# Kernel optimization log

Hardware: AMD Instinct MI355X
Metric: run time of the kernel (lower is better)

Reference implementation:

```python
import jax, jax.numpy as jnp
import numpy as np

HEADS = 8

def setup_inputs() -> dict:
    key = jax.random.key(0)
    ks = jax.random.split(key, 6)
    N, C, L = 8, 512, 2048
    s = 0.02
    return {
        'x':  jax.random.normal(ks[0], (N, C, L), dtype=jnp.float32),
        'Wq': jax.random.normal(ks[1], (C, C), dtype=jnp.float32) * s,
        'Wk': jax.random.normal(ks[2], (C, C), dtype=jnp.float32) * s,
        'Wv': jax.random.normal(ks[3], (C, C), dtype=jnp.float32) * s,
        'Wo': jax.random.normal(ks[4], (C, C), dtype=jnp.float32) * s,
        'bo': jnp.zeros((C,), dtype=jnp.float32),
    }

def reference(x, Wq, Wk, Wv, Wo, bo):
    N, C, L = x.shape
    h = HEADS
    d = C // h
    scale = C ** (-0.5)  # note: scales by full channels, as in the original

    def proj(W):
        # Conv1d(k=1, bias=False) == per-position linear: [N,C,L] -> [N,L,h,d]
        y = jnp.einsum('oc,ncl->nlo', W, x)
        return y.reshape(N, L, h, d)

    q, k, v = proj(Wq), proj(Wk), proj(Wv)

    qk = jnp.einsum('nqhd,nkhd->nhqk', q, k)  # [N,h,L,L]
    causal_mask = jnp.tril(jnp.ones((L, L), dtype=bool))
    qk = jnp.where(causal_mask, qk, -jnp.inf)
    attn = jax.nn.softmax(qk * scale, axis=-1)

    out = jnp.einsum('nhqk,nkhd->nqhd', attn, v)  # [N,L,h,d]
    out = out.reshape(N, L, C).transpose(0, 2, 1)  # n (h d) l
    return jnp.einsum('oc,ncl->nol', Wo, out) + bo[None, :, None]
```

## Files before the change

### kernel.cpp

```cpp
#include <hip/hip_runtime.h>
#include <math.h>

typedef __bf16 bf16;
typedef __attribute__((ext_vector_type(8))) __bf16 bf16x8;
typedef __attribute__((ext_vector_type(4))) float f32x4;
typedef __attribute__((ext_vector_type(16))) float f32x16;
typedef unsigned short u16;
typedef unsigned int u32;

constexpr int Nn = 8, Cc = 512, Ll = 2048, Hh = 8, Dd = 64;
constexpr float kScale = 0.044194173824159216f;
constexpr float kQexp2 = kScale * 1.44269504088896341f;
constexpr size_t NCL = (size_t)Nn * Cc * Ll;
constexpr size_t WSZ = (size_t)Cc * Cc;

static __device__ __forceinline__ u16 bfbits(bf16 v) {
    union { bf16 b; u16 u; } x; x.b = v; return x.u;
}
static __device__ __forceinline__ float fexp2(float x) {
#if __has_builtin(__builtin_amdgcn_exp2f)
    return __builtin_amdgcn_exp2f(x);
#else
    return exp2f(x);
#endif
}

#define MFMA(a, b, c) __builtin_amdgcn_mfma_f32_16x16x32_bf16((a), (b), (c), 0, 0, 0)
#define MFMA32(a, b, c) __builtin_amdgcn_mfma_f32_32x32x16_bf16((a), (b), (c), 0, 0, 0)

static __device__ __forceinline__ void async16(const bf16* g, bf16* l) {
    __builtin_amdgcn_global_load_lds(
        (const __attribute__((address_space(1))) void*)g,
        (__attribute__((address_space(3))) void*)l, 16, 0, 0);
}

static __device__ __forceinline__ u32 cvtpk(float lo, float hi) {
    u32 d;
    asm("v_cvt_pk_bf16_f32 %0, %1, %2" : "=v"(d) : "v"(lo), "v"(hi));
    return d;
}
static __device__ __forceinline__ void swap32(u32& d, u32& s) {
    asm volatile("v_permlane32_swap_b32 %0, %1" : "+v"(d), "+v"(s));
}

__global__ __launch_bounds__(256) void prep_kernel(
    const float* __restrict__ x,
    const float* __restrict__ Wq, const float* __restrict__ Wk,
    const float* __restrict__ Wv, const float* __restrict__ Wo,
    bf16* __restrict__ xT, bf16* __restrict__ Wb)
{
    const int tid = threadIdx.x;
    if (blockIdx.z == Nn) {
        int gid = (blockIdx.y * 32 + blockIdx.x) * 256 + tid;
        int w = gid >> 14;
        int o = (gid & 16383) * 4;
        const float* src = (w == 0) ? Wq : (w == 1) ? Wk : (w == 2) ? Wv : Wo;
        bf16* dst = Wb + (size_t)w * WSZ;
#pragma unroll
        for (int j = 0; j < 4; j++) {
            float4 v = ((const float4*)src)[o + j];
            ushort4 u;
            u.x = bfbits((bf16)v.x); u.y = bfbits((bf16)v.y);
            u.z = bfbits((bf16)v.z); u.w = bfbits((bf16)v.w);
            *(ushort4*)(dst + (size_t)(o + j) * 4) = u;
        }
        return;
    }

    __shared__ bf16 Ts[64][72];
    const int lt = blockIdx.x, ct = blockIdx.y, n = blockIdx.z;

    const int cr = tid >> 2, l0 = (tid & 3) * 16;
    const float* src = x + ((size_t)(n * Cc + ct * 64 + cr)) * Ll + lt * 64 + l0;
#pragma unroll
    for (int i = 0; i < 4; i++) {
        float4 v = *(const float4*)(src + i * 4);
        Ts[l0 + i * 4 + 0][cr] = (bf16)v.x;
        Ts[l0 + i * 4 + 1][cr] = (bf16)v.y;
        Ts[l0 + i * 4 + 2][cr] = (bf16)v.z;
        Ts[l0 + i * 4 + 3][cr] = (bf16)v.w;
    }
    __syncthreads();

    const int lr = tid >> 2, c0 = (tid & 3) * 16;
    bf16* dst = xT + ((size_t)(n * Ll + lt * 64 + lr)) * Cc + ct * 64 + c0;
    *(bf16x8*)(dst)     = *(const bf16x8*)&Ts[lr][c0];
    *(bf16x8*)(dst + 8) = *(const bf16x8*)&Ts[lr][c0 + 8];
}

__global__ __launch_bounds__(256) void qkv_gemm(
    const bf16* __restrict__ xT, const bf16* __restrict__ Wb,
    bf16* __restrict__ Qt, bf16* __restrict__ Kt, bf16* __restrict__ Vb)
{
    const int lt = blockIdx.x, ow = blockIdx.y, n = blockIdx.z;
    const int widx = ow >> 2, otile = ow & 3;

    __shared__ bf16 Xs[128 * 64];
    __shared__ bf16 Ws[128 * 64];

    const int tid = threadIdx.x;
    const int lane = tid & 63, wv = tid >> 6;
    const int m = lane & 15, quad = lane >> 4;
    const int rh = wv & 1, ch = wv >> 1;

    const bf16* __restrict__ W = Wb + (size_t)widx * WSZ + (size_t)otile * 128 * Cc;
    const bf16* __restrict__ X = xT + (size_t)(n * Ll + lt * 128) * Cc;

    int srow[4], scol[4];
#pragma unroll
    for (int i = 0; i < 4; i++) {
        int q = i * 256 + tid;
        srow[i] = q >> 3;
        scol[i] = ((q ^ (q >> 3)) & 7) * 8;
    }

    f32x4 acc[4][4] = {};

    for (int c0 = 0; c0 < Cc; c0 += 64) {
#pragma unroll
        for (int i = 0; i < 4; i++)
            async16(&X[(size_t)srow[i] * Cc + c0 + scol[i]], &Xs[(i * 256 + tid) * 8]);
#pragma unroll
        for (int i = 0; i < 4; i++)
            async16(&W[(size_t)srow[i] * Cc + c0 + scol[i]], &Ws[(i * 256 + tid) * 8]);
        __syncthreads();

        const bf16* TA = (widx < 2) ? Xs : Ws;
        const bf16* TB = (widx < 2) ? Ws : Xs;
#pragma unroll
        for (int kk = 0; kk < 2; kk++) {
            const int sw = (((kk * 4 + quad) ^ (m & 7)) * 8);
            bf16x8 af[4], bfr[4];
#pragma unroll
            for (int t = 0; t < 4; t++)
                af[t] = *(const bf16x8*)&TA[(rh * 64 + t * 16 + m) * 64 + sw];
#pragma unroll
            for (int u = 0; u < 4; u++)
                bfr[u] = *(const bf16x8*)&TB[(ch * 64 + u * 16 + m) * 64 + sw];
#pragma unroll
            for (int t = 0; t < 4; t++)
#pragma unroll
                for (int u = 0; u < 4; u++)
                    acc[t][u] = MFMA(af[t], bfr[u], acc[t][u]);
        }
        __syncthreads();
    }

    if (widx < 2) {
        const float fq = (widx == 0) ? kQexp2 : 1.0f;
        bf16* __restrict__ OUT = (widx == 0) ? Qt : Kt;
#pragma unroll
        for (int u = 0; u < 4; u++) {
            const int o = otile * 128 + ch * 64 + u * 16 + m;
            const int h = o >> 6, d = o & 63;
            bf16* base = OUT + (size_t)(n * Hh + h) * Ll * Dd + d;
#pragma unroll
            for (int t = 0; t < 4; t++) {
                const int l0 = lt * 128 + rh * 64 + t * 16 + quad * 4;
#pragma unroll
                for (int r = 0; r < 4; r++)
                    base[(size_t)(l0 + r) * Dd] = (bf16)(acc[t][u][r] * fq);
            }
        }
    } else {
#pragma unroll
        for (int t = 0; t < 4; t++) {
            const int ob = otile * 128 + rh * 64 + t * 16 + quad * 4;
#pragma unroll
            for (int r = 0; r < 4; r++) {
                const int oo = ob + r, h = oo >> 6, d = oo & 63;
                bf16* base = Vb + ((size_t)(n * Hh + h) * Dd + d) * Ll;
#pragma unroll
                for (int u = 0; u < 4; u++)
                    base[lt * 128 + ch * 64 + u * 16 + m] = (bf16)acc[t][u][r];
            }
        }
    }
}

__global__ __launch_bounds__(256, 4) void attn_mfma(
    const bf16* __restrict__ Qt, const bf16* __restrict__ Kt,
    const bf16* __restrict__ Vb, bf16* __restrict__ AO)
{
    const int h  = blockIdx.x;
    const int jp = blockIdx.y;
    const int n  = blockIdx.z;

    __shared__ bf16 KV[2][2][64 * 64];
    __shared__ float Lsc[4][64];

    const int tid = threadIdx.x;
    const int lane = tid & 63, wv = tid >> 6;
    const int l31 = lane & 31, hb = lane >> 5;
    const int sw7 = l31 & 7;

    const size_t bnh = (size_t)(n * Hh + h) * Ll * Dd;
    const bf16* __restrict__ Qh = Qt + bnh;
    const bf16* __restrict__ Kh = Kt + bnh;
    const bf16* __restrict__ Vh = Vb + bnh;

    const int srow = tid >> 3;
    const int scs  = (((tid & 7) ^ (srow & 7)) * 8);
    const int mhalf = wv & 1;

#pragma unroll 1
    for (int ph = 0; ph < 2; ph++) {
        const int st = ph ? (15 - jp) : jp;
        const int nk = 2 * st + 2;
        const int dtile = 2 * st + (wv >> 1);
        const int qrow0 = st * 128 + wv * 32;

        bf16x8 qf[4];
#pragma unroll
        for (int s = 0; s < 4; s++)
            qf[s] = *(const bf16x8*)&Qh[(size_t)(qrow0 + l31) * Dd + s * 16 + hb * 8];

        f32x16 O0 = {}, O1 = {};
        float Lacc = 0.f;

        async16(&Kh[(size_t)srow * Dd + scs],        &KV[0][0][(size_t)tid * 8]);
        async16(&Kh[(size_t)(srow + 32) * Dd + scs], &KV[0][0][(size_t)tid * 8 + 2048]);
        async16(&Vh[(size_t)srow * Ll + scs],        &KV[0][1][(size_t)tid * 8]);
        async16(&Vh[(size_t)(srow + 32) * Ll + scs], &KV[0][1][(size_t)tid * 8 + 2048]);
        __syncthreads();

        for (int kt = 0; kt < nk; kt++) {
            const int cur = kt & 1;

            if (kt + 1 < nk) {
                const int kn = (kt + 1) * 64;
                async16(&Kh[(size_t)(kn + srow) * Dd + scs],      &KV[cur ^ 1][0][(size_t)tid * 8]);
                async16(&Kh[(size_t)(kn + srow + 32) * Dd + scs], &KV[cur ^ 1][0][(size_t)tid * 8 + 2048]);
                async16(&Vh[(size_t)srow * Ll + kn + scs],        &KV[cur ^ 1][1][(size_t)tid * 8]);
                async16(&Vh[(size_t)(srow + 32) * Ll + kn + scs], &KV[cur ^ 1][1][(size_t)tid * 8 + 2048]);
            }

            if (kt <= dtile) {
                const bf16* Ks = &KV[cur][0][0];
                const bf16* Vs = &KV[cur][1][0];
                const bool dg = (kt == dtile);

#pragma unroll
                for (int i = 0; i < 2; i++) {
                    if (i == 1 && dg && mhalf == 0) continue;

                    f32x16 St = {};
#pragma unroll
                    for (int s = 0; s < 4; s++) {
                        bf16x8 kfs = *(const bf16x8*)
                            &Ks[(32 * i + l31) * 64 + (((2 * s + hb) ^ sw7) * 8)];
                        St = MFMA32(kfs, qf[s], St);
                    }

                    const bool msk = dg && (i == mhalf);

#pragma unroll
                    for (int s = 0; s < 2; s++) {
                        const int c0 = 4 * i + 2 * s + hb;
                        bf16x8 v0 = *(const bf16x8*)&Vs[l31 * 64 + ((c0 ^ sw7) * 8)];
                        bf16x8 v1 = *(const bf16x8*)&Vs[(32 + l31) * 64 + ((c0 ^ sw7) * 8)];

                        float p[8];
#pragma unroll
                        for (int j = 0; j < 8; j++) {
                            const int r = s * 8 + j;
                            float pv = fexp2(St[r]);
                            if (msk) {
                                const int kc = (r & 3) + 8 * (r >> 2) + 4 * hb;
                                if (kc > l31) pv = 0.f;
                            }
                            p[j] = pv;
                        }
                        Lacc += ((p[0] + p[1]) + (p[2] + p[3]))
                              + ((p[4] + p[5]) + (p[6] + p[7]));

                        u32 A = cvtpk(p[0], p[1]);
                        u32 B = cvtpk(p[2], p[3]);
                        u32 C = cvtpk(p[4], p[5]);
                        u32 D = cvtpk(p[6], p[7]);
                        swap32(A, C);
                        swap32(B, D);
                        union { u32 w[4]; bf16x8 v; } pu;
                        pu.w[0] = A; pu.w[1] = B; pu.w[2] = C; pu.w[3] = D;

                        O0 = MFMA32(pu.v, v0, O0);
                        O1 = MFMA32(pu.v, v1, O1);
                    }
                }
            }

            __syncthreads();
        }

        {
            Lsc[wv][hb * 32 + l31] = Lacc;
            const float a  = Lsc[wv][l31];
            const float b  = Lsc[wv][32 + l31];
            const float Lt = a + b;
            Lsc[wv][l31] = Lt;

            const size_t aobase = (size_t)n * Ll * Cc + (size_t)h * 64;
#pragma unroll
            for (int r = 0; r < 16; r++) {
                const int qr = (r & 3) + 8 * (r >> 2) + 4 * hb;
                const float inv = 1.0f / Lsc[wv][qr];
                const size_t row = aobase + (size_t)(qrow0 + qr) * Cc;
                AO[row + l31]      = (bf16)(O0[r] * inv);
                AO[row + 32 + l31] = (bf16)(O1[r] * inv);
            }
        }
    }
}

__global__ __launch_bounds__(256) void out_gemm(
    const bf16* __restrict__ AO, const bf16* __restrict__ Wb,
    const float* __restrict__ bo, float* __restrict__ out)
{
    const int lt = blockIdx.x, ot = blockIdx.y, n = blockIdx.z;

    __shared__ bf16 Ws[128 * 64];
    __shared__ bf16 Bs[128 * 64];

    const int tid = threadIdx.x;
    const int lane = tid & 63, wv = tid >> 6;
    const int m = lane & 15, quad = lane >> 4;
    const int rh = wv & 1, ch = wv >> 1;

    const bf16* __restrict__ W = Wb + 3 * WSZ + (size_t)ot * 128 * Cc;
    const bf16* __restrict__ B = AO + (size_t)(n * Ll + lt * 128) * Cc;

    int srow[4], scol[4];
#pragma unroll
    for (int i = 0; i < 4; i++) {
        int q = i * 256 + tid;
        srow[i] = q >> 3;
        scol[i] = ((q ^ (q >> 3)) & 7) * 8;
    }

    f32x4 acc[4][4] = {};

    for (int c0 = 0; c0 < Cc; c0 += 64) {
#pragma unroll
        for (int i = 0; i < 4; i++)
            async16(&W[(size_t)srow[i] * Cc + c0 + scol[i]], &Ws[(i * 256 + tid) * 8]);
#pragma unroll
        for (int i = 0; i < 4; i++)
            async16(&B[(size_t)srow[i] * Cc + c0 + scol[i]], &Bs[(i * 256 + tid) * 8]);
        __syncthreads();

#pragma unroll
        for (int kk = 0; kk < 2; kk++) {
            const int sw = (((kk * 4 + quad) ^ (m & 7)) * 8);
            bf16x8 af[4], bfr[4];
#pragma unroll
            for (int t = 0; t < 4; t++)
                af[t] = *(const bf16x8*)&Ws[(rh * 64 + t * 16 + m) * 64 + sw];
#pragma unroll
            for (int u = 0; u < 4; u++)
                bfr[u] = *(const bf16x8*)&Bs[(ch * 64 + u * 16 + m) * 64 + sw];
#pragma unroll
            for (int t = 0; t < 4; t++)
#pragma unroll
                for (int u = 0; u < 4; u++)
                    acc[t][u] = MFMA(af[t], bfr[u], acc[t][u]);
        }
        __syncthreads();
    }

#pragma unroll
    for (int t = 0; t < 4; t++) {
        const int ob = ot * 128 + rh * 64 + t * 16 + quad * 4;
#pragma unroll
        for (int r = 0; r < 4; r++) {
            const int o = ob + r;
            const float b = bo[o];
            float* base = out + ((size_t)n * Cc + o) * Ll + lt * 128 + ch * 64;
#pragma unroll
            for (int u = 0; u < 4; u++)
                base[u * 16 + m] = acc[t][u][r] + b;
        }
    }
}

extern "C" void kernel_launch(void* const* d_in, const int* in_sizes, int n_in,
                              void* d_out, int out_size, void* d_ws, size_t ws_size,
                              hipStream_t stream)
{
    const float* x  = (const float*)d_in[0];
    const float* Wq = (const float*)d_in[1];
    const float* Wk = (const float*)d_in[2];
    const float* Wv = (const float*)d_in[3];
    const float* Wo = (const float*)d_in[4];
    const float* bo = (const float*)d_in[5];
    float* out = (float*)d_out;

    bf16* ws = (bf16*)d_ws;
    bf16* xT = ws;
    bf16* Wb = xT + NCL;
    bf16* Qt = Wb + 4 * WSZ;
    bf16* Kt = Qt + NCL;
    bf16* Vb = Kt + NCL;
    bf16* AO = Vb + NCL;

    prep_kernel<<<dim3(32, 8, Nn + 1), 256, 0, stream>>>(x, Wq, Wk, Wv, Wo, xT, Wb);
    qkv_gemm<<<dim3(16, 12, Nn), 256, 0, stream>>>(xT, Wb, Qt, Kt, Vb);
    attn_mfma<<<dim3(Hh, 8, Nn), 256, 0, stream>>>(Qt, Kt, Vb, AO);
    out_gemm<<<dim3(16, 4, Nn), 256, 0, stream>>>(AO, Wb, bo, out);
}
```

Before: 191.2 us.

## Enlarge attention query tile to 256 rows, two 32-row groups per wave

```diff
diff --git a/kernel.cpp b/kernel.cpp
--- a/kernel.cpp
+++ b/kernel.cpp
@@ -41,6 +41,33 @@
 }
 static __device__ __forceinline__ void swap32(u32& d, u32& s) {
     asm volatile("v_permlane32_swap_b32 %0, %1" : "+v"(d), "+v"(s));
+}
+
+template<int S>
+static __device__ __forceinline__ bf16x8 packP(const f32x16 St, bool msk,
+                                               int hb, int l31, float& La)
+{
+    float p[8];
+#pragma unroll
+    for (int j = 0; j < 8; j++) {
+        const int r = S * 8 + j;
+        float pv = fexp2(St[r]);
+        if (msk) {
+            const int kc = (r & 3) + 8 * (r >> 2) + 4 * hb;
+            if (kc > l31) pv = 0.f;
+        }
+        p[j] = pv;
+    }
+    La += ((p[0] + p[1]) + (p[2] + p[3])) + ((p[4] + p[5]) + (p[6] + p[7]));
+    u32 A = cvtpk(p[0], p[1]);
+    u32 B = cvtpk(p[2], p[3]);
+    u32 C = cvtpk(p[4], p[5]);
+    u32 D = cvtpk(p[6], p[7]);
+    swap32(A, C);
+    swap32(B, D);
+    union { u32 w[4]; bf16x8 v; } pu;
+    pu.w[0] = A; pu.w[1] = B; pu.w[2] = C; pu.w[3] = D;
+    return pu.v;
 }
 
 __global__ __launch_bounds__(256) void prep_kernel(
@@ -178,7 +205,7 @@
     }
 }
 
-__global__ __launch_bounds__(256, 4) void attn_mfma(
+__global__ __launch_bounds__(256, 1) void attn_mfma(
     const bf16* __restrict__ Qt, const bf16* __restrict__ Kt,
     const bf16* __restrict__ Vb, bf16* __restrict__ AO)
 {
@@ -187,7 +214,7 @@
     const int n  = blockIdx.z;
 
     __shared__ bf16 KV[2][2][64 * 64];
-    __shared__ float Lsc[4][64];
+    __shared__ float Lsc[4][2][64];
 
     const int tid = threadIdx.x;
     const int lane = tid & 63, wv = tid >> 6;
@@ -201,22 +228,24 @@
 
     const int srow = tid >> 3;
     const int scs  = (((tid & 7) ^ (srow & 7)) * 8);
-    const int mhalf = wv & 1;
 
 #pragma unroll 1
     for (int ph = 0; ph < 2; ph++) {
-        const int st = ph ? (15 - jp) : jp;
-        const int nk = 2 * st + 2;
-        const int dtile = 2 * st + (wv >> 1);
-        const int qrow0 = st * 128 + wv * 32;
-
-        bf16x8 qf[4];
-#pragma unroll
-        for (int s = 0; s < 4; s++)
-            qf[s] = *(const bf16x8*)&Qh[(size_t)(qrow0 + l31) * Dd + s * 16 + hb * 8];
-
-        f32x16 O0 = {}, O1 = {};
-        float Lacc = 0.f;
+        const int st = ph ? (7 - jp) : jp;
+        const int nk = 4 * st + 4;
+        const int dtile = 4 * st + wv;
+        const int qbase = st * 256 + wv * 64;
+
+        bf16x8 qf[2][4];
+#pragma unroll
+        for (int g = 0; g < 2; g++)
+#pragma unroll
+            for (int s = 0; s < 4; s++)
+                qf[g][s] = *(const bf16x8*)
+                    &Qh[(size_t)(qbase + 32 * g + l31) * Dd + s * 16 + hb * 8];
+
+        f32x16 O00 = {}, O01 = {}, O10 = {}, O11 = {};
+        float La0 = 0.f, La1 = 0.f;
 
         async16(&Kh[(size_t)srow * Dd + scs],        &KV[0][0][(size_t)tid * 8]);
         async16(&Kh[(size_t)(srow + 32) * Dd + scs], &KV[0][0][(size_t)tid * 8 + 2048]);
@@ -242,49 +271,53 @@
 
 #pragma unroll
                 for (int i = 0; i < 2; i++) {
-                    if (i == 1 && dg && mhalf == 0) continue;
-
-                    f32x16 St = {};
+                    const bool skip0 = dg && (i == 1);
+
+                    bf16x8 kf[4];
+#pragma unroll
+                    for (int s = 0; s < 4; s++)
+                        kf[s] = *(const bf16x8*)
+                            &Ks[(32 * i + l31) * 64 + (((2 * s + hb) ^ sw7) * 8)];
+
+                    f32x16 St0 = {}, St1 = {};
 #pragma unroll
                     for (int s = 0; s < 4; s++) {
-                        bf16x8 kfs = *(const bf16x8*)
-                            &Ks[(32 * i + l31) * 64 + (((2 * s + hb) ^ sw7) * 8)];
-                        St = MFMA32(kfs, qf[s], St);
+                        if (!skip0) St0 = MFMA32(kf[s], qf[0][s], St0);
+                        St1 = MFMA32(kf[s], qf[1][s], St1);
                     }
 
-                    const bool msk = dg && (i == mhalf);
-
-#pragma unroll
-                    for (int s = 0; s < 2; s++) {
-                        const int c0 = 4 * i + 2 * s + hb;
+                    const bool m0 = dg && (i == 0);
+                    const bool m1 = dg && (i == 1);
+
+                    {
+                        const int c0 = 4 * i + 0 + hb;
                         bf16x8 v0 = *(const bf16x8*)&Vs[l31 * 64 + ((c0 ^ sw7) * 8)];
                         bf16x8 v1 = *(const bf16x8*)&Vs[(32 + l31) * 64 + ((c0 ^ sw7) * 8)];
-
-                        float p[8];
-#pragma unroll
-                        for (int j = 0; j < 8; j++) {
-                            const int r = s * 8 + j;
-                            float pv = fexp2(St[r]);
-                            if (msk) {
-                                const int kc = (r & 3) + 8 * (r >> 2) + 4 * hb;
-                                if (kc > l31) pv = 0.f;
-                            }
-                            p[j] = pv;
+                        if (!skip0) {
+                            bf16x8 pu = packP<0>(St0, m0, hb, l31, La0);
+                            O00 = MFMA32(pu, v0, O00);
+                            O01 = MFMA32(pu, v1, O01);
                         }
-                        Lacc += ((p[0] + p[1]) + (p[2] + p[3]))
-                              + ((p[4] + p[5]) + (p[6] + p[7]));
-
-                        u32 A = cvtpk(p[0], p[1]);
-                        u32 B = cvtpk(p[2], p[3]);
-                        u32 C = cvtpk(p[4], p[5]);
-                        u32 D = cvtpk(p[6], p[7]);
-                        swap32(A, C);
-                        swap32(B, D);
-                        union { u32 w[4]; bf16x8 v; } pu;
-                        pu.w[0] = A; pu.w[1] = B; pu.w[2] = C; pu.w[3] = D;
-
-                        O0 = MFMA32(pu.v, v0, O0);
-                        O1 = MFMA32(pu.v, v1, O1);
+                        {
+                            bf16x8 pu = packP<0>(St1, m1, hb, l31, La1);
+                            O10 = MFMA32(pu, v0, O10);
+                            O11 = MFMA32(pu, v1, O11);
+                        }
+                    }
+                    {
+                        const int c0 = 4 * i + 2 + hb;
+                        bf16x8 v0 = *(const bf16x8*)&Vs[l31 * 64 + ((c0 ^ sw7) * 8)];
+                        bf16x8 v1 = *(const bf16x8*)&Vs[(32 + l31) * 64 + ((c0 ^ sw7) * 8)];
+                        if (!skip0) {
+                            bf16x8 pu = packP<1>(St0, m0, hb, l31, La0);
+                            O00 = MFMA32(pu, v0, O00);
+                            O01 = MFMA32(pu, v1, O01);
+                        }
+                        {
+                            bf16x8 pu = packP<1>(St1, m1, hb, l31, La1);
+                            O10 = MFMA32(pu, v0, O10);
+                            O11 = MFMA32(pu, v1, O11);
+                        }
                     }
                 }
             }
@@ -293,21 +326,26 @@
         }
 
         {
-            Lsc[wv][hb * 32 + l31] = Lacc;
-            const float a  = Lsc[wv][l31];
-            const float b  = Lsc[wv][32 + l31];
-            const float Lt = a + b;
-            Lsc[wv][l31] = Lt;
+            Lsc[wv][0][hb * 32 + l31] = La0;
+            Lsc[wv][1][hb * 32 + l31] = La1;
+            const float t0 = Lsc[wv][0][l31] + Lsc[wv][0][32 + l31];
+            const float t1 = Lsc[wv][1][l31] + Lsc[wv][1][32 + l31];
+            Lsc[wv][0][l31] = t0;
+            Lsc[wv][1][l31] = t1;
 
             const size_t aobase = (size_t)n * Ll * Cc + (size_t)h * 64;
 #pragma unroll
-            for (int r = 0; r < 16; r++) {
-                const int qr = (r & 3) + 8 * (r >> 2) + 4 * hb;
-                const float inv = 1.0f / Lsc[wv][qr];
-                const size_t row = aobase + (size_t)(qrow0 + qr) * Cc;
-                AO[row + l31]      = (bf16)(O0[r] * inv);
-                AO[row + 32 + l31] = (bf16)(O1[r] * inv);
-            }
+            for (int g = 0; g < 2; g++)
+#pragma unroll
+                for (int r = 0; r < 16; r++) {
+                    const int qr = (r & 3) + 8 * (r >> 2) + 4 * hb;
+                    const float inv = 1.0f / Lsc[wv][g][qr];
+                    const size_t row = aobase + (size_t)(qbase + 32 * g + qr) * Cc;
+                    const float o0 = (g == 0) ? O00[r] : O10[r];
+                    const float o1 = (g == 0) ? O01[r] : O11[r];
+                    AO[row + l31]      = (bf16)(o0 * inv);
+                    AO[row + 32 + l31] = (bf16)(o1 * inv);
+                }
         }
     }
 }
@@ -404,6 +442,6 @@
 
     prep_kernel<<<dim3(32, 8, Nn + 1), 256, 0, stream>>>(x, Wq, Wk, Wv, Wo, xT, Wb);
     qkv_gemm<<<dim3(16, 12, Nn), 256, 0, stream>>>(xT, Wb, Qt, Kt, Vb);
-    attn_mfma<<<dim3(Hh, 8, Nn), 256, 0, stream>>>(Qt, Kt, Vb, AO);
+    attn_mfma<<<dim3(Hh, 4, Nn), 256, 0, stream>>>(Qt, Kt, Vb, AO);
     out_gemm<<<dim3(16, 4, Nn), 256, 0, stream>>>(AO, Wb, bo, out);
 }
```

After: 209.8 us. +9.7%, slower.
